# Kernel optimization log

Measured on AMD Instinct MI355X. Metric: run time of the kernel, lower is better.

## Reference

```python
import jax, jax.numpy as jnp
import numpy as np

N_NODES = 100000
N_EDGES = 1250000
D_IN = 64
D_OUT = 64


def setup_inputs() -> dict:
    key = jax.random.key(0)
    k_h, k_e, k_src, k_dst, k_w, k_b = jax.random.split(key, 6)
    h = jax.random.normal(k_h, (N_NODES, D_IN), dtype=jnp.float32)
    e = jax.random.normal(k_e, (N_EDGES, 1), dtype=jnp.float32)
    src = jax.random.randint(k_src, (N_EDGES,), 0, N_NODES, dtype=jnp.int64)
    dst = jax.random.randint(k_dst, (N_EDGES,), 0, N_NODES, dtype=jnp.int64)
    W = jax.random.normal(k_w, (D_OUT, D_IN), dtype=jnp.float32) / np.sqrt(D_IN)
    b = jax.random.normal(k_b, (D_OUT,), dtype=jnp.float32) * 0.01
    return {"h": h, "e": e, "src": src, "dst": dst, "W": W, "b": b}


def reference(h, e, src, dst, W, b):
    # u_mul_e: gather source node features and multiply by edge features [E,1] -> [E,D]
    m = h[src] * e
    # fn.sum('m','ft'): scatter-add messages into destination nodes -> [N,D]
    ft = jax.ops.segment_sum(m, dst, num_segments=N_NODES)
    # nn.Linear(input_dim, output_dim)
    return ft @ W.T + b
```

## Files before the change

kernel.cpp:

```cpp
#include <hip/hip_runtime.h>

#define N_NODES 100000
#define N_EDGES 1250000
#define D 64
#define BUCKET_BITS 6
#define BUCKET_SZ 64
#define NBUCK 1563
#define CAP 1024
#define EPT 16
#define EPB (EPT * 256)
#define BIN_BLOCKS ((N_EDGES + EPB - 1) / EPB)
#define TR_BLOCKS ((N_NODES + 63) / 64)
#define FUSED_BLOCKS (TR_BLOCKS + BIN_BLOCKS)


typedef __attribute__((ext_vector_type(8))) short bf16x8;
typedef __attribute__((ext_vector_type(4))) float f32x4;

__device__ __forceinline__ unsigned bf16_rne(float x) {
    unsigned u = __float_as_uint(x);
    return (u + 0x7FFFu + ((u >> 16) & 1u)) >> 16;
}
__device__ __forceinline__ float bf16_to_f(unsigned short v) {
    return __uint_as_float(((unsigned)v) << 16);
}

__device__ __forceinline__ void bf16_split(float x, short& hi, short& lo) {
    unsigned hb = bf16_rne(x);
    float fh = __uint_as_float(hb << 16);
    hi = (short)hb;
    lo = (short)bf16_rne(x - fh);
}

__global__ __launch_bounds__(256) void transform_bin_kernel(const float* __restrict__ h,
                                                            const float* __restrict__ W,
                                                            unsigned short* __restrict__ g16,
                                                            const int* __restrict__ src,
                                                            const int* __restrict__ dst,
                                                            const float* __restrict__ e,
                                                            int* __restrict__ gcursor,
                                                            int2* __restrict__ packed) {
    __shared__ __align__(16) char smem_raw[8192];

    int t = threadIdx.x;
    int bx = blockIdx.x;
    int cb = bx / 6;
    bool is_bin = ((bx % 6) == 5) && (cb < BIN_BLOCKS);
    int nbin_before = (cb < BIN_BLOCKS) ? cb : BIN_BLOCKS;

    if (!is_bin) {
        unsigned short* sh = (unsigned short*)smem_raw;
        int trb = bx - nbin_before;
        int lane = t & 63;
        int w = t >> 6;
        int li = lane & 15;
        int lg = lane >> 4;
        int nodebase = trb * 64 + w * 16;

        bf16x8 bhi[4][2], blo[4][2];
#pragma unroll
        for (int nt = 0; nt < 4; ++nt) {
#pragma unroll
            for (int kk = 0; kk < 2; ++kk) {
                const float* wp = W + (nt * 16 + li) * D + kk * 32 + lg * 8;
                float4 w0 = *(const float4*)wp;
                float4 w1 = *(const float4*)(wp + 4);
                float v[8] = {w0.x, w0.y, w0.z, w0.w, w1.x, w1.y, w1.z, w1.w};
                bf16x8 h8, l8;
#pragma unroll
                for (int q = 0; q < 8; ++q) { short a, b; bf16_split(v[q], a, b); h8[q] = a; l8[q] = b; }
                bhi[nt][kk] = h8;
                blo[nt][kk] = l8;
            }
        }

        int arow = nodebase + li;
        if (arow > N_NODES - 1) arow = N_NODES - 1;
        bf16x8 ahi[2], alo[2];
#pragma unroll
        for (int kk = 0; kk < 2; ++kk) {
            const float* hp = h + (long)arow * D + kk * 32 + lg * 8;
            float4 h0 = *(const float4*)hp;
            float4 h1 = *(const float4*)(hp + 4);
            float v[8] = {h0.x, h0.y, h0.z, h0.w, h1.x, h1.y, h1.z, h1.w};
            bf16x8 h8, l8;
#pragma unroll
            for (int q = 0; q < 8; ++q) { short a, b; bf16_split(v[q], a, b); h8[q] = a; l8[q] = b; }
            ahi[kk] = h8;
            alo[kk] = l8;
        }

        f32x4 acc[4];
#pragma unroll
        for (int nt = 0; nt < 4; ++nt) acc[nt] = (f32x4){0.f, 0.f, 0.f, 0.f};
#pragma unroll
        for (int kk = 0; kk < 2; ++kk) {
#pragma unroll
            for (int nt = 0; nt < 4; ++nt) {
                acc[nt] = __builtin_amdgcn_mfma_f32_16x16x32_bf16(ahi[kk], bhi[nt][kk], acc[nt], 0, 0, 0);
                acc[nt] = __builtin_amdgcn_mfma_f32_16x16x32_bf16(ahi[kk], blo[nt][kk], acc[nt], 0, 0, 0);
                acc[nt] = __builtin_amdgcn_mfma_f32_16x16x32_bf16(alo[kk], bhi[nt][kk], acc[nt], 0, 0, 0);
            }
        }

#pragma unroll
        for (int nt = 0; nt < 4; ++nt) {
#pragma unroll
            for (int r = 0; r < 4; ++r) {
                sh[(w * 16 + lg * 4 + r) * D + nt * 16 + li] = (unsigned short)bf16_rne(acc[nt][r]);
            }
        }
        __syncthreads();

        const uint4* s4 = (const uint4*)sh;
        uint4* g4 = (uint4*)(g16 + (long)trb * 64 * D);
#pragma unroll
        for (int i = t; i < 512; i += 256) {
            int n = trb * 64 + (i >> 3);
            if (n < N_NODES) g4[i] = s4[i];
        }
    } else {
        int* lhist = (int*)smem_raw;
        for (int j = t; j < NBUCK; j += 256) lhist[j] = 0;
        __syncthreads();

        int b[EPT], r[EPT], sv[EPT];
        float ev[EPT];
        int base = cb * EPB;
#pragma unroll
        for (int j = 0; j < EPT; ++j) {
            int i = base + j * 256 + t;
            b[j] = -1;
            if (i < N_EDGES) {
                int d = dst[i];
                b[j] = d >> BUCKET_BITS;
                sv[j] = src[i] | ((d & (BUCKET_SZ - 1)) << 20);
                ev[j] = e[i];
                r[j] = atomicAdd(&lhist[b[j]], 1);
            }
        }
        __syncthreads();

        for (int x = t; x < NBUCK; x += 256) {
            int c = lhist[x];
            lhist[x] = (c > 0) ? atomicAdd(&gcursor[x], c) : 0;
        }
        __syncthreads();

#pragma unroll
        for (int j = 0; j < EPT; ++j) {
            if (b[j] >= 0) {
                int pos = lhist[b[j]] + r[j];
                if (pos < CAP) packed[b[j] * CAP + pos] = make_int2(sv[j], __float_as_int(ev[j]));
            }
        }
    }
}

__global__ __launch_bounds__(512) void gather_bucket_kernel(const unsigned short* __restrict__ g16,
                                                            const int2* __restrict__ packed,
                                                            const int* __restrict__ gcursor,
                                                            const float* __restrict__ bias,
                                                            float* __restrict__ out) {
    __shared__ int2 eds[CAP];
    __shared__ int nhist[BUCKET_SZ];
    __shared__ int nbase[BUCKET_SZ];
    __shared__ int ncur[BUCKET_SZ];

    int t = threadIdx.x;
    int bk = blockIdx.x;
    int start = bk * CAP;
    int cnt = gcursor[bk];
    if (cnt > CAP) cnt = CAP;

    if (t < BUCKET_SZ) nhist[t] = 0;
    __syncthreads();

    int2 pa = make_int2(0, 0), pb = pa;
    bool va = t < cnt, vb = t + 512 < cnt;
    if (va) pa = packed[start + t];
    if (vb) pb = packed[start + t + 512];
    if (va) atomicAdd(&nhist[(pa.x >> 20) & (BUCKET_SZ - 1)], 1);
    if (vb) atomicAdd(&nhist[(pb.x >> 20) & (BUCKET_SZ - 1)], 1);
    __syncthreads();

    if (t < BUCKET_SZ) {
        int c = nhist[t];
        int v = c;
#pragma unroll
        for (int off = 1; off < BUCKET_SZ; off <<= 1) {
            int x = __shfl_up(v, off, 64);
            if (t >= off) v += x;
        }
        nbase[t] = v - c;
        ncur[t] = v - c;
    }
    __syncthreads();

    if (va) { int dl = (pa.x >> 20) & (BUCKET_SZ - 1); eds[atomicAdd(&ncur[dl], 1)] = pa; }
    if (vb) { int dl = (pb.x >> 20) & (BUCKET_SZ - 1); eds[atomicAdd(&ncur[dl], 1)] = pb; }
    __syncthreads();

    int w = t >> 6;
    int lane = t & 63;
    float bv = bias[lane];
    for (int jj = 0; jj < 8; ++jj) {
        int n = w * 8 + jj;
        int gn = bk * BUCKET_SZ + n;
        int s = nbase[n];
        int c = nhist[n];
        float acc = bv;
        int k = 0;
        for (; k + 8 <= c; k += 8) {
            int2 q0 = eds[s + k + 0], q1 = eds[s + k + 1];
            int2 q2 = eds[s + k + 2], q3 = eds[s + k + 3];
            int2 q4 = eds[s + k + 4], q5 = eds[s + k + 5];
            int2 q6 = eds[s + k + 6], q7 = eds[s + k + 7];
            float g0 = bf16_to_f(g16[(long)(q0.x & 0xFFFFF) * D + lane]);
            float g1 = bf16_to_f(g16[(long)(q1.x & 0xFFFFF) * D + lane]);
            float g2 = bf16_to_f(g16[(long)(q2.x & 0xFFFFF) * D + lane]);
            float g3 = bf16_to_f(g16[(long)(q3.x & 0xFFFFF) * D + lane]);
            float g4 = bf16_to_f(g16[(long)(q4.x & 0xFFFFF) * D + lane]);
            float g5 = bf16_to_f(g16[(long)(q5.x & 0xFFFFF) * D + lane]);
            float g6 = bf16_to_f(g16[(long)(q6.x & 0xFFFFF) * D + lane]);
            float g7 = bf16_to_f(g16[(long)(q7.x & 0xFFFFF) * D + lane]);
            acc += __int_as_float(q0.y) * g0;
            acc += __int_as_float(q1.y) * g1;
            acc += __int_as_float(q2.y) * g2;
            acc += __int_as_float(q3.y) * g3;
            acc += __int_as_float(q4.y) * g4;
            acc += __int_as_float(q5.y) * g5;
            acc += __int_as_float(q6.y) * g6;
            acc += __int_as_float(q7.y) * g7;
        }
        if (k + 4 <= c) {
            int2 q0 = eds[s + k + 0], q1 = eds[s + k + 1];
            int2 q2 = eds[s + k + 2], q3 = eds[s + k + 3];
            float g0 = bf16_to_f(g16[(long)(q0.x & 0xFFFFF) * D + lane]);
            float g1 = bf16_to_f(g16[(long)(q1.x & 0xFFFFF) * D + lane]);
            float g2 = bf16_to_f(g16[(long)(q2.x & 0xFFFFF) * D + lane]);
            float g3 = bf16_to_f(g16[(long)(q3.x & 0xFFFFF) * D + lane]);
            acc += __int_as_float(q0.y) * g0;
            acc += __int_as_float(q1.y) * g1;
            acc += __int_as_float(q2.y) * g2;
            acc += __int_as_float(q3.y) * g3;
            k += 4;
        }
        for (; k < c; ++k) {
            int2 q = eds[s + k];
            acc += __int_as_float(q.y) * bf16_to_f(g16[(long)(q.x & 0xFFFFF) * D + lane]);
        }
        if (gn < N_NODES) out[(long)gn * D + lane] = acc;
    }
}

extern "C" void kernel_launch(void* const* d_in, const int* in_sizes, int n_in,
                              void* d_out, int out_size, void* d_ws, size_t ws_size,
                              hipStream_t stream) {
    const float* h   = (const float*)d_in[0];
    const float* e   = (const float*)d_in[1];
    const int*   src = (const int*)d_in[2];
    const int*   dst = (const int*)d_in[3];
    const float* W   = (const float*)d_in[4];
    const float* b   = (const float*)d_in[5];
    float* out = (float*)d_out;

    char* ws = (char*)d_ws;
    int2*           packed  = (int2*)          (ws);
    int*            gcursor = (int*)           (ws + 12804096);
    unsigned short* g16     = (unsigned short*)(ws + 12810368);

    hipMemsetAsync(gcursor, 0, NBUCK * sizeof(int), stream);

    transform_bin_kernel<<<FUSED_BLOCKS, 256, 0, stream>>>(h, W, g16, src, dst, e, gcursor, packed);

    gather_bucket_kernel<<<NBUCK, 512, 0, stream>>>(g16, packed, gcursor, b, out);
}
```

Before: 154.9 us.

## Process two node tiles per transform block and two-pass the binning to cut registers

Each transform block now handles 128 nodes as two 64-node tiles, prefetching both h rows up front. W is reloaded and split inside the MFMA loop instead of being held in registers, which lowers register pressure. The block interleave changes from 5:1 to 2:1 transform:bin. The binning blocks no longer keep per-edge state in registers; they re-read dst/src/e in a second pass and use a shared cursor array for slots, trading extra global reads and LDS atomics for lower register use and higher occupancy.

```diff
diff --git a/kernel.cpp b/kernel.cpp
--- a/kernel.cpp
+++ b/kernel.cpp
@@ -10,7 +10,7 @@
 #define EPT 16
 #define EPB (EPT * 256)
 #define BIN_BLOCKS ((N_EDGES + EPB - 1) / EPB)
-#define TR_BLOCKS ((N_NODES + 63) / 64)
+#define TR_BLOCKS 782
 #define FUSED_BLOCKS (TR_BLOCKS + BIN_BLOCKS)
 
 
@@ -30,6 +30,53 @@
     float fh = __uint_as_float(hb << 16);
     hi = (short)hb;
     lo = (short)bf16_rne(x - fh);
+}
+
+__device__ __forceinline__ void transform_tile(float4 hk0a, float4 hk0b,
+                                               float4 hk1a, float4 hk1b,
+                                               const float* __restrict__ W,
+                                               unsigned short* __restrict__ sh,
+                                               int li, int lg, int w) {
+    bf16x8 ahi[2], alo[2];
+    {
+        float av[8] = {hk0a.x, hk0a.y, hk0a.z, hk0a.w, hk0b.x, hk0b.y, hk0b.z, hk0b.w};
+#pragma unroll
+        for (int q = 0; q < 8; ++q) { short a, b; bf16_split(av[q], a, b); ahi[0][q] = a; alo[0][q] = b; }
+    }
+    {
+        float av[8] = {hk1a.x, hk1a.y, hk1a.z, hk1a.w, hk1b.x, hk1b.y, hk1b.z, hk1b.w};
+#pragma unroll
+        for (int q = 0; q < 8; ++q) { short a, b; bf16_split(av[q], a, b); ahi[1][q] = a; alo[1][q] = b; }
+    }
+
+    f32x4 acc[4];
+#pragma unroll
+    for (int nt = 0; nt < 4; ++nt) acc[nt] = (f32x4){0.f, 0.f, 0.f, 0.f};
+
+#pragma unroll
+    for (int kk = 0; kk < 2; ++kk) {
+#pragma unroll
+        for (int nt = 0; nt < 4; ++nt) {
+            const float* wp = W + (nt * 16 + li) * D + kk * 32 + lg * 8;
+            float4 w0 = *(const float4*)wp;
+            float4 w1 = *(const float4*)(wp + 4);
+            float bv[8] = {w0.x, w0.y, w0.z, w0.w, w1.x, w1.y, w1.z, w1.w};
+            bf16x8 bhi, blo;
+#pragma unroll
+            for (int q = 0; q < 8; ++q) { short a, b; bf16_split(bv[q], a, b); bhi[q] = a; blo[q] = b; }
+            acc[nt] = __builtin_amdgcn_mfma_f32_16x16x32_bf16(ahi[kk], bhi, acc[nt], 0, 0, 0);
+            acc[nt] = __builtin_amdgcn_mfma_f32_16x16x32_bf16(ahi[kk], blo, acc[nt], 0, 0, 0);
+            acc[nt] = __builtin_amdgcn_mfma_f32_16x16x32_bf16(alo[kk], bhi, acc[nt], 0, 0, 0);
+        }
+    }
+
+#pragma unroll
+    for (int nt = 0; nt < 4; ++nt) {
+#pragma unroll
+        for (int r = 0; r < 4; ++r) {
+            sh[(w * 16 + lg * 4 + r) * D + nt * 16 + li] = (unsigned short)bf16_rne(acc[nt][r]);
+        }
+    }
 }
 
 __global__ __launch_bounds__(256) void transform_bin_kernel(const float* __restrict__ h,
@@ -40,104 +87,75 @@
                                                             const float* __restrict__ e,
                                                             int* __restrict__ gcursor,
                                                             int2* __restrict__ packed) {
-    __shared__ __align__(16) char smem_raw[8192];
+    __shared__ __align__(16) char smem_raw[16384];
 
     int t = threadIdx.x;
     int bx = blockIdx.x;
-    int cb = bx / 6;
-    bool is_bin = ((bx % 6) == 5) && (cb < BIN_BLOCKS);
-    int nbin_before = (cb < BIN_BLOCKS) ? cb : BIN_BLOCKS;
+    bool is_bin = ((bx % 3) == 2) && (bx / 3 < BIN_BLOCKS);
 
     if (!is_bin) {
-        unsigned short* sh = (unsigned short*)smem_raw;
-        int trb = bx - nbin_before;
+        int nb = (bx + 1) / 3; if (nb > BIN_BLOCKS) nb = BIN_BLOCKS;
+        int trb = bx - nb;
         int lane = t & 63;
         int w = t >> 6;
         int li = lane & 15;
         int lg = lane >> 4;
-        int nodebase = trb * 64 + w * 16;
-
-        bf16x8 bhi[4][2], blo[4][2];
-#pragma unroll
-        for (int nt = 0; nt < 4; ++nt) {
-#pragma unroll
-            for (int kk = 0; kk < 2; ++kk) {
-                const float* wp = W + (nt * 16 + li) * D + kk * 32 + lg * 8;
-                float4 w0 = *(const float4*)wp;
-                float4 w1 = *(const float4*)(wp + 4);
-                float v[8] = {w0.x, w0.y, w0.z, w0.w, w1.x, w1.y, w1.z, w1.w};
-                bf16x8 h8, l8;
-#pragma unroll
-                for (int q = 0; q < 8; ++q) { short a, b; bf16_split(v[q], a, b); h8[q] = a; l8[q] = b; }
-                bhi[nt][kk] = h8;
-                blo[nt][kk] = l8;
+
+        int base0 = trb * 128 + w * 16;
+        int base1 = base0 + 64;
+        int arow0 = base0 + li; if (arow0 > N_NODES - 1) arow0 = N_NODES - 1;
+        int arow1 = base1 + li; if (arow1 > N_NODES - 1) arow1 = N_NODES - 1;
+
+        const float* hp0 = h + (long)arow0 * D + lg * 8;
+        const float* hp1 = h + (long)arow1 * D + lg * 8;
+        float4 a0k0a = *(const float4*)(hp0);
+        float4 a0k0b = *(const float4*)(hp0 + 4);
+        float4 a0k1a = *(const float4*)(hp0 + 32);
+        float4 a0k1b = *(const float4*)(hp0 + 36);
+        float4 a1k0a = *(const float4*)(hp1);
+        float4 a1k0b = *(const float4*)(hp1 + 4);
+        float4 a1k1a = *(const float4*)(hp1 + 32);
+        float4 a1k1b = *(const float4*)(hp1 + 36);
+
+        unsigned short* sh0 = (unsigned short*)smem_raw;
+        unsigned short* sh1 = sh0 + 64 * D;
+
+        transform_tile(a0k0a, a0k0b, a0k1a, a0k1b, W, sh0, li, lg, w);
+        __syncthreads();
+        {
+            const uint4* s4 = (const uint4*)sh0;
+            uint4* g4 = (uint4*)(g16 + (long)base0 * 0 + (long)(trb * 128) * D);
+#pragma unroll
+            for (int i = t; i < 512; i += 256) {
+                int n = trb * 128 + (i >> 3);
+                if (n < N_NODES) g4[i] = s4[i];
             }
         }
 
-        int arow = nodebase + li;
-        if (arow > N_NODES - 1) arow = N_NODES - 1;
-        bf16x8 ahi[2], alo[2];
-#pragma unroll
-        for (int kk = 0; kk < 2; ++kk) {
-            const float* hp = h + (long)arow * D + kk * 32 + lg * 8;
-            float4 h0 = *(const float4*)hp;
-            float4 h1 = *(const float4*)(hp + 4);
-            float v[8] = {h0.x, h0.y, h0.z, h0.w, h1.x, h1.y, h1.z, h1.w};
-            bf16x8 h8, l8;
-#pragma unroll
-            for (int q = 0; q < 8; ++q) { short a, b; bf16_split(v[q], a, b); h8[q] = a; l8[q] = b; }
-            ahi[kk] = h8;
-            alo[kk] = l8;
-        }
-
-        f32x4 acc[4];
-#pragma unroll
-        for (int nt = 0; nt < 4; ++nt) acc[nt] = (f32x4){0.f, 0.f, 0.f, 0.f};
-#pragma unroll
-        for (int kk = 0; kk < 2; ++kk) {
-#pragma unroll
-            for (int nt = 0; nt < 4; ++nt) {
-                acc[nt] = __builtin_amdgcn_mfma_f32_16x16x32_bf16(ahi[kk], bhi[nt][kk], acc[nt], 0, 0, 0);
-                acc[nt] = __builtin_amdgcn_mfma_f32_16x16x32_bf16(ahi[kk], blo[nt][kk], acc[nt], 0, 0, 0);
-                acc[nt] = __builtin_amdgcn_mfma_f32_16x16x32_bf16(alo[kk], bhi[nt][kk], acc[nt], 0, 0, 0);
+        transform_tile(a1k0a, a1k0b, a1k1a, a1k1b, W, sh1, li, lg, w);
+        __syncthreads();
+        {
+            const uint4* s4 = (const uint4*)sh1;
+            uint4* g4 = (uint4*)(g16 + (long)(trb * 128 + 64) * D);
+#pragma unroll
+            for (int i = t; i < 512; i += 256) {
+                int n = trb * 128 + 64 + (i >> 3);
+                if (n < N_NODES) g4[i] = s4[i];
             }
-        }
-
-#pragma unroll
-        for (int nt = 0; nt < 4; ++nt) {
-#pragma unroll
-            for (int r = 0; r < 4; ++r) {
-                sh[(w * 16 + lg * 4 + r) * D + nt * 16 + li] = (unsigned short)bf16_rne(acc[nt][r]);
-            }
-        }
-        __syncthreads();
-
-        const uint4* s4 = (const uint4*)sh;
-        uint4* g4 = (uint4*)(g16 + (long)trb * 64 * D);
-#pragma unroll
-        for (int i = t; i < 512; i += 256) {
-            int n = trb * 64 + (i >> 3);
-            if (n < N_NODES) g4[i] = s4[i];
         }
     } else {
         int* lhist = (int*)smem_raw;
-        for (int j = t; j < NBUCK; j += 256) lhist[j] = 0;
-        __syncthreads();
-
-        int b[EPT], r[EPT], sv[EPT];
-        float ev[EPT];
+        int* lcur  = lhist + NBUCK;
+        int cb = bx / 3;
         int base = cb * EPB;
-#pragma unroll
+
+        for (int j = t; j < NBUCK; j += 256) { lhist[j] = 0; lcur[j] = 0; }
+        __syncthreads();
+
+#pragma unroll 4
         for (int j = 0; j < EPT; ++j) {
             int i = base + j * 256 + t;
-            b[j] = -1;
-            if (i < N_EDGES) {
-                int d = dst[i];
-                b[j] = d >> BUCKET_BITS;
-                sv[j] = src[i] | ((d & (BUCKET_SZ - 1)) << 20);
-                ev[j] = e[i];
-                r[j] = atomicAdd(&lhist[b[j]], 1);
-            }
+            if (i < N_EDGES) atomicAdd(&lhist[dst[i] >> BUCKET_BITS], 1);
         }
         __syncthreads();
 
@@ -147,11 +165,16 @@
         }
         __syncthreads();
 
-#pragma unroll
+#pragma unroll 4
         for (int j = 0; j < EPT; ++j) {
-            if (b[j] >= 0) {
-                int pos = lhist[b[j]] + r[j];
-                if (pos < CAP) packed[b[j] * CAP + pos] = make_int2(sv[j], __float_as_int(ev[j]));
+            int i = base + j * 256 + t;
+            if (i < N_EDGES) {
+                int d = dst[i];
+                int bk = d >> BUCKET_BITS;
+                int pos = lhist[bk] + atomicAdd(&lcur[bk], 1);
+                if (pos < CAP)
+                    packed[bk * CAP + pos] = make_int2(src[i] | ((d & (BUCKET_SZ - 1)) << 20),
+                                                       __float_as_int(e[i]));
             }
         }
     }
```

New measurement: 163.5 us. 5.6% more time.

## Restructure binning into two-pass histogram and interleave transform/bin blocks differently

Applied to the files above, without the earlier changes.

Binning blocks now handle twice as many edges each and no longer keep per-edge bucket, rank, src and e values in registers. Instead they count the destination histogram in a first pass, then re-read dst/src/e and take ranks from a second shared-memory cursor array. The global-cursor reservation loop is rotated per block to spread atomic contention, and the bin/transform interleave ratio is changed to match. The transform path converts W to bf16 hi/lo inside the MFMA loop rather than holding all of W in registers up front, which lowers register pressure. In exchange, edge inputs are read twice and the extra shared cursor atomics make within-bucket ordering nondeterministic.

```diff
diff --git a/kernel.cpp b/kernel.cpp
--- a/kernel.cpp
+++ b/kernel.cpp
@@ -7,11 +7,12 @@
 #define BUCKET_SZ 64
 #define NBUCK 1563
 #define CAP 1024
-#define EPT 16
+#define EPT 32
 #define EPB (EPT * 256)
 #define BIN_BLOCKS ((N_EDGES + EPB - 1) / EPB)
 #define TR_BLOCKS ((N_NODES + 63) / 64)
 #define FUSED_BLOCKS (TR_BLOCKS + BIN_BLOCKS)
+#define STRIDE 11
 
 
 typedef __attribute__((ext_vector_type(8))) short bf16x8;
@@ -40,66 +41,52 @@
                                                             const float* __restrict__ e,
                                                             int* __restrict__ gcursor,
                                                             int2* __restrict__ packed) {
-    __shared__ __align__(16) char smem_raw[8192];
+    __shared__ __align__(16) char smem_raw[12544];
 
     int t = threadIdx.x;
     int bx = blockIdx.x;
-    int cb = bx / 6;
-    bool is_bin = ((bx % 6) == 5) && (cb < BIN_BLOCKS);
-    int nbin_before = (cb < BIN_BLOCKS) ? cb : BIN_BLOCKS;
+    bool is_bin = ((bx % STRIDE) == (STRIDE - 1)) && (bx / STRIDE < BIN_BLOCKS);
 
     if (!is_bin) {
         unsigned short* sh = (unsigned short*)smem_raw;
-        int trb = bx - nbin_before;
+        int nb = (bx + 1) / STRIDE; if (nb > BIN_BLOCKS) nb = BIN_BLOCKS;
+        int trb = bx - nb;
         int lane = t & 63;
         int w = t >> 6;
         int li = lane & 15;
         int lg = lane >> 4;
         int nodebase = trb * 64 + w * 16;
 
-        bf16x8 bhi[4][2], blo[4][2];
-#pragma unroll
-        for (int nt = 0; nt < 4; ++nt) {
-#pragma unroll
-            for (int kk = 0; kk < 2; ++kk) {
-                const float* wp = W + (nt * 16 + li) * D + kk * 32 + lg * 8;
-                float4 w0 = *(const float4*)wp;
-                float4 w1 = *(const float4*)(wp + 4);
-                float v[8] = {w0.x, w0.y, w0.z, w0.w, w1.x, w1.y, w1.z, w1.w};
-                bf16x8 h8, l8;
-#pragma unroll
-                for (int q = 0; q < 8; ++q) { short a, b; bf16_split(v[q], a, b); h8[q] = a; l8[q] = b; }
-                bhi[nt][kk] = h8;
-                blo[nt][kk] = l8;
-            }
-        }
-
         int arow = nodebase + li;
         if (arow > N_NODES - 1) arow = N_NODES - 1;
-        bf16x8 ahi[2], alo[2];
+
+        f32x4 acc[4];
+#pragma unroll
+        for (int nt = 0; nt < 4; ++nt) acc[nt] = (f32x4){0.f, 0.f, 0.f, 0.f};
+
 #pragma unroll
         for (int kk = 0; kk < 2; ++kk) {
             const float* hp = h + (long)arow * D + kk * 32 + lg * 8;
             float4 h0 = *(const float4*)hp;
             float4 h1 = *(const float4*)(hp + 4);
-            float v[8] = {h0.x, h0.y, h0.z, h0.w, h1.x, h1.y, h1.z, h1.w};
-            bf16x8 h8, l8;
-#pragma unroll
-            for (int q = 0; q < 8; ++q) { short a, b; bf16_split(v[q], a, b); h8[q] = a; l8[q] = b; }
-            ahi[kk] = h8;
-            alo[kk] = l8;
-        }
-
-        f32x4 acc[4];
-#pragma unroll
-        for (int nt = 0; nt < 4; ++nt) acc[nt] = (f32x4){0.f, 0.f, 0.f, 0.f};
-#pragma unroll
-        for (int kk = 0; kk < 2; ++kk) {
+            float av[8] = {h0.x, h0.y, h0.z, h0.w, h1.x, h1.y, h1.z, h1.w};
+            bf16x8 ahi, alo;
+#pragma unroll
+            for (int q = 0; q < 8; ++q) { short a, b; bf16_split(av[q], a, b); ahi[q] = a; alo[q] = b; }
+
 #pragma unroll
             for (int nt = 0; nt < 4; ++nt) {
-                acc[nt] = __builtin_amdgcn_mfma_f32_16x16x32_bf16(ahi[kk], bhi[nt][kk], acc[nt], 0, 0, 0);
-                acc[nt] = __builtin_amdgcn_mfma_f32_16x16x32_bf16(ahi[kk], blo[nt][kk], acc[nt], 0, 0, 0);
-                acc[nt] = __builtin_amdgcn_mfma_f32_16x16x32_bf16(alo[kk], bhi[nt][kk], acc[nt], 0, 0, 0);
+                const float* wp = W + (nt * 16 + li) * D + kk * 32 + lg * 8;
+                float4 w0 = *(const float4*)wp;
+                float4 w1 = *(const float4*)(wp + 4);
+                float bv[8] = {w0.x, w0.y, w0.z, w0.w, w1.x, w1.y, w1.z, w1.w};
+                bf16x8 bhi, blo;
+#pragma unroll
+                for (int q = 0; q < 8; ++q) { short a, b; bf16_split(bv[q], a, b); bhi[q] = a; blo[q] = b; }
+
+                acc[nt] = __builtin_amdgcn_mfma_f32_16x16x32_bf16(ahi, bhi, acc[nt], 0, 0, 0);
+                acc[nt] = __builtin_amdgcn_mfma_f32_16x16x32_bf16(ahi, blo, acc[nt], 0, 0, 0);
+                acc[nt] = __builtin_amdgcn_mfma_f32_16x16x32_bf16(alo, bhi, acc[nt], 0, 0, 0);
             }
         }
 
@@ -121,37 +108,40 @@
         }
     } else {
         int* lhist = (int*)smem_raw;
-        for (int j = t; j < NBUCK; j += 256) lhist[j] = 0;
-        __syncthreads();
-
-        int b[EPT], r[EPT], sv[EPT];
-        float ev[EPT];
+        int* lcur  = lhist + NBUCK;
+        int cb = bx / STRIDE;
         int base = cb * EPB;
-#pragma unroll
+
+        for (int j = t; j < NBUCK; j += 256) { lhist[j] = 0; lcur[j] = 0; }
+        __syncthreads();
+
+#pragma unroll 8
         for (int j = 0; j < EPT; ++j) {
             int i = base + j * 256 + t;
-            b[j] = -1;
+            if (i < N_EDGES) atomicAdd(&lhist[dst[i] >> BUCKET_BITS], 1);
+        }
+        __syncthreads();
+
+        {
+            int rot = (cb * 521) % NBUCK;
+            for (int x = t; x < NBUCK; x += 256) {
+                int xi = x + rot; if (xi >= NBUCK) xi -= NBUCK;
+                int c = lhist[xi];
+                lhist[xi] = (c > 0) ? atomicAdd(&gcursor[xi], c) : 0;
+            }
+        }
+        __syncthreads();
+
+#pragma unroll 8
+        for (int j = 0; j < EPT; ++j) {
+            int i = base + j * 256 + t;
             if (i < N_EDGES) {
                 int d = dst[i];
-                b[j] = d >> BUCKET_BITS;
-                sv[j] = src[i] | ((d & (BUCKET_SZ - 1)) << 20);
-                ev[j] = e[i];
-                r[j] = atomicAdd(&lhist[b[j]], 1);
-            }
-        }
-        __syncthreads();
-
-        for (int x = t; x < NBUCK; x += 256) {
-            int c = lhist[x];
-            lhist[x] = (c > 0) ? atomicAdd(&gcursor[x], c) : 0;
-        }
-        __syncthreads();
-
-#pragma unroll
-        for (int j = 0; j < EPT; ++j) {
-            if (b[j] >= 0) {
-                int pos = lhist[b[j]] + r[j];
-                if (pos < CAP) packed[b[j] * CAP + pos] = make_int2(sv[j], __float_as_int(ev[j]));
+                int bk = d >> BUCKET_BITS;
+                int pos = lhist[bk] + atomicAdd(&lcur[bk], 1);
+                if (pos < CAP)
+                    packed[bk * CAP + pos] = make_int2(src[i] | ((d & (BUCKET_SZ - 1)) << 20),
+                                                       __float_as_int(e[i]));
             }
         }
     }
```

Result: slower. 185.4 us (+19.7%).
